# Performance work log

Measured on AMD Instinct MI355X. Metric: run time of the kernel, lower is better.

The kernel has to match this reference:

```python
import jax, jax.numpy as jnp
import numpy as np
from jax import lax

B, S, D, H = 4, 1024, 1024, 16
DK = D // H


def setup_inputs() -> dict:
    key = jax.random.key(0)
    ks = jax.random.split(key, 8)
    s = 0.02
    return {
        "text_embeddings": jax.random.normal(ks[0], (B, S, D), jnp.float32),
        "text_mask": jnp.ones((B, S), jnp.int32),
        "W_G": jax.random.normal(ks[1], (D, D), jnp.float32) * s,
        "b_G": jnp.zeros((D,), jnp.float32),
        "Wq": jax.random.normal(ks[2], (D, D), jnp.float32) * s,
        "bq": jnp.zeros((D,), jnp.float32),
        "Wk": jax.random.normal(ks[3], (D, D), jnp.float32) * s,
        "bk": jnp.zeros((D,), jnp.float32),
        "conv_w": jax.random.normal(ks[4], (D, H, 3), jnp.float32) * s,
        "conv_b": jnp.zeros((D,), jnp.float32),
    }


def _rope_tables(seq_len, dk):
    # interleaved sinusoidal tables, each value repeated twice along feature dim
    pos = jnp.arange(seq_len, dtype=jnp.float32)[:, None]            # [S,1]
    inv = jnp.power(10000.0, -2.0 * jnp.arange(dk // 2, dtype=jnp.float32) / dk)
    ang = pos * inv                                                   # [S,DK/2]
    cos_pos = jnp.repeat(jnp.cos(ang), 2, axis=-1)[None, None]        # [1,1,S,DK]
    sin_pos = jnp.repeat(jnp.sin(ang), 2, axis=-1)[None, None]
    return cos_pos, sin_pos


def reference(text_embeddings, text_mask, W_G, b_G, Wq, bq, Wk, bk, conv_w, conv_b):
    b, s, d = text_embeddings.shape
    g = text_embeddings @ W_G + b_G                                   # [B,S,D]
    q = (g @ Wq + bq).reshape(b, s, H, DK).transpose(0, 2, 1, 3)      # [B,H,S,DK]
    k = (g @ Wk + bk).reshape(b, s, H, DK).transpose(0, 2, 1, 3)

    cos_pos, sin_pos = _rope_tables(s, DK)
    # NOTE: query rotation uses +q_odd (module does NOT negate for q), key uses -k_odd
    qw2 = jnp.stack([q[..., 1::2], q[..., ::2]], axis=-1).reshape(q.shape)
    qw = q * cos_pos + qw2 * sin_pos
    kw2 = jnp.stack([-k[..., 1::2], k[..., ::2]], axis=-1).reshape(k.shape)
    kw = k * cos_pos + kw2 * sin_pos

    scores = jnp.einsum("bhqd,bhkd->bhqk", qw, kw) / np.float32(np.sqrt(DK))
    mask = text_mask[:, None, None, :]                                # [B,1,1,S]
    scores = jnp.where(mask == 0, jnp.float32(-1e9), scores)
    p_attn = jax.nn.softmax(scores, axis=-1)                          # [B,H,S,S]

    row0 = p_attn[:, :, 0, :]                                         # [B,H,S]
    conv = lax.conv_general_dilated(
        row0, conv_w, window_strides=(1,), padding=[(1, 1)],
        dimension_numbers=("NCH", "OIH", "NCH"))                      # [B,D,S]
    return jax.nn.relu(conv + conv_b[None, :, None])
```

## Files before the change

kernel.cpp:

```cpp
#include <hip/hip_runtime.h>
#include <math.h>

#define B_  4
#define S_  1024
#define D_  1024
#define H_  16
#define DK_ 64
#define M_  (B_ * S_)

typedef __bf16 bf16x8 __attribute__((ext_vector_type(8)));
typedef float  f32x4  __attribute__((ext_vector_type(4)));

__device__ __forceinline__ unsigned short f2bf(float f) {
  unsigned u = __builtin_bit_cast(unsigned, f);
  u = (u + 0x7FFFu + ((u >> 16) & 1u)) >> 16;
  return (unsigned short)u;
}
__device__ __forceinline__ float bf2f(unsigned short h) {
  unsigned u = ((unsigned)h) << 16;
  return __builtin_bit_cast(float, u);
}

__device__ __forceinline__ void gl_lds16(const void* g, void* lds) {
  __builtin_amdgcn_global_load_lds(
      (const __attribute__((address_space(1))) unsigned int*)(unsigned long long)g,
      (__attribute__((address_space(3))) unsigned int*)(unsigned int)(unsigned long long)lds,
      16, 0, 0);
}

__global__ __launch_bounds__(256) void prep_kernel(
    const float* __restrict__ X, const float* __restrict__ W_G,
    const float* __restrict__ Wk, unsigned short* __restrict__ Xbf,
    unsigned short* __restrict__ WGT, unsigned short* __restrict__ WkT,
    float* __restrict__ tab) {
  __shared__ float tle[32][33];
  const int blk = blockIdx.x;
  const int tid = threadIdx.x;

  if (blk < 2048) {
    const int i = (blk * 256 + tid) * 2;
    const float4 v0 = ((const float4*)X)[i];
    const float4 v1 = ((const float4*)X)[i + 1];
    ushort4 h0, h1;
    h0.x = f2bf(v0.x); h0.y = f2bf(v0.y); h0.z = f2bf(v0.z); h0.w = f2bf(v0.w);
    h1.x = f2bf(v1.x); h1.y = f2bf(v1.y); h1.z = f2bf(v1.z); h1.w = f2bf(v1.w);
    ((ushort4*)Xbf)[i] = h0;
    ((ushort4*)Xbf)[i + 1] = h1;
  } else if (blk < 4096) {
    const bool isG = blk < 3072;
    const float* W = isG ? W_G : Wk;
    unsigned short* WT = isG ? WGT : WkT;
    const int t = isG ? blk - 2048 : blk - 3072;
    const int k0 = (t & 31) * 32;
    const int n0 = (t >> 5) * 32;
    const int tx = tid & 31;
    const int ty = tid >> 5;
#pragma unroll
    for (int r = 0; r < 32; r += 8)
      tle[ty + r][tx] = W[(size_t)(k0 + ty + r) * 1024 + n0 + tx];
    __syncthreads();
#pragma unroll
    for (int r = 0; r < 32; r += 8)
      WT[(size_t)(n0 + ty + r) * 1024 + k0 + tx] = f2bf(tle[tx][ty + r]);
  } else {
    const int idx = (blk - 4096) * 256 + tid;
    const int s = idx >> 5, j = idx & 31;
    const float inv = (float)exp(-(double)j * (9.210340371976182736 / 32.0));
    float sn, c;
    sincosf((float)s * inv, &sn, &c);
    tab[(size_t)s * 64 + 2 * j] = c;
    tab[(size_t)s * 64 + 2 * j + 1] = sn;
  }
}

#define GM 64
#define GN 128

__global__ __launch_bounds__(256) void gemm_bf16(
    const unsigned short* __restrict__ A, const unsigned short* __restrict__ BT,
    const float* __restrict__ bias, unsigned short* __restrict__ C,
    const float* __restrict__ Wq, float* __restrict__ part, int nGemmBlocks) {
  __shared__ __align__(16) unsigned short As[2][GM * 32];
  __shared__ __align__(16) unsigned short Bs[2][GN * 32];
  __shared__ float gs[4][32];

  const int flat = blockIdx.x;
  const int tid  = threadIdx.x;

  if (flat >= nGemmBlocks) {
    const int qb = flat - nGemmBlocks;
    const int slab = qb >> 2;
    const int n = (qb & 3) * 256 + tid;
    if (tid < 128) {
      const int b = tid >> 5, kk = tid & 31;
      gs[b][kk] = bf2f(A[(size_t)b * S_ * D_ + slab * 32 + kk]);
    }
    __syncthreads();
    float a0 = 0.f, a1 = 0.f, a2 = 0.f, a3 = 0.f;
#pragma unroll
    for (int kk = 0; kk < 32; ++kk) {
      const float w = Wq[(size_t)(slab * 32 + kk) * D_ + n];
      a0 = fmaf(gs[0][kk], w, a0);
      a1 = fmaf(gs[1][kk], w, a1);
      a2 = fmaf(gs[2][kk], w, a2);
      a3 = fmaf(gs[3][kk], w, a3);
    }
    part[(size_t)(slab * 4 + 0) * D_ + n] = a0;
    part[(size_t)(slab * 4 + 1) * D_ + n] = a1;
    part[(size_t)(slab * 4 + 2) * D_ + n] = a2;
    part[(size_t)(slab * 4 + 3) * D_ + n] = a3;
    return;
  }

  const int bx = flat >> 6;
  const int by = flat & 63;
  const int wv   = tid >> 6;
  const int lane = tid & 63;
  const int m0 = by * GM;
  const int n0 = bx * GN;

  const int colOff = (lane & 3) * 8;
  const size_t aOff  = (size_t)(m0 + 16 * wv + (lane >> 2)) * 1024 + colOff;
  const size_t bOff0 = (size_t)(n0 + 32 * wv + (lane >> 2)) * 1024 + colOff;
  const size_t bOff1 = bOff0 + (size_t)16 * 1024;

  const int l15  = lane & 15;
  const int quad = lane >> 4;

  f32x4 acc[4][2];
#pragma unroll
  for (int i = 0; i < 4; ++i)
#pragma unroll
    for (int j = 0; j < 2; ++j) acc[i][j] = (f32x4){0.f, 0.f, 0.f, 0.f};

#pragma unroll 1
  for (int k0 = 0; k0 < 1024; k0 += 64) {
    __syncthreads();
#pragma unroll
    for (int ks = 0; ks < 2; ++ks) {
      gl_lds16(A  + aOff  + k0 + ks * 32, &As[ks][wv * 512]);
      gl_lds16(BT + bOff0 + k0 + ks * 32, &Bs[ks][wv * 1024]);
      gl_lds16(BT + bOff1 + k0 + ks * 32, &Bs[ks][wv * 1024 + 512]);
    }
    __syncthreads();

#pragma unroll
    for (int ks = 0; ks < 2; ++ks) {
      bf16x8 af[4], bfr[2];
#pragma unroll
      for (int mi = 0; mi < 4; ++mi)
        af[mi] = *(const bf16x8*)(&As[ks][(mi * 16 + l15) * 32 + quad * 8]);
#pragma unroll
      for (int ni = 0; ni < 2; ++ni)
        bfr[ni] =
            *(const bf16x8*)(&Bs[ks][(wv * 32 + ni * 16 + l15) * 32 + quad * 8]);
#pragma unroll
      for (int mi = 0; mi < 4; ++mi)
#pragma unroll
        for (int ni = 0; ni < 2; ++ni)
          acc[mi][ni] = __builtin_amdgcn_mfma_f32_16x16x32_bf16(
              af[mi], bfr[ni], acc[mi][ni], 0, 0, 0);
    }
  }

#pragma unroll
  for (int ni = 0; ni < 2; ++ni) {
    const int n = n0 + wv * 32 + ni * 16 + l15;
    const float bv = bias[n];
#pragma unroll
    for (int mi = 0; mi < 4; ++mi) {
#pragma unroll
      for (int r = 0; r < 4; ++r) {
        const int m = m0 + mi * 16 + quad * 4 + r;
        C[(size_t)m * 1024 + n] = f2bf(acc[mi][ni][r] + bv);
      }
    }
  }
}

__global__ __launch_bounds__(256) void attn_scores_kernel(
    const unsigned short* __restrict__ Kbf, const float* __restrict__ part,
    const float* __restrict__ bq, const float* __restrict__ tab,
    const int* __restrict__ mask, float* __restrict__ scores,
    float* __restrict__ mS) {
  const int bi = blockIdx.x;
  const int b = bi >> 9;
  const int h = (bi >> 5) & 15;
  const int chunk = bi & 31;
  const int tid = threadIdx.x;
  const int bh = b * H_ + h;
  const int sl = tid >> 3;
  const int j  = tid & 7;
  const int s  = chunk * 32 + sl;

  __shared__ float q0s[DK_];
  __shared__ float wredm[4];
  __shared__ float wreds[4];

  if (tid < 64) {
    const int n = h * DK_ + tid;
    float v = bq[n];
#pragma unroll
    for (int sl2 = 0; sl2 < 32; ++sl2)
      v += part[(size_t)(sl2 * 4 + b) * D_ + n];
    q0s[tid] = v;
  }
  __syncthreads();

  const ushort4* kp =
      (const ushort4*)(Kbf + ((size_t)(b * S_ + s)) * D_ + h * DK_ + j * 8);
  const ushort4 k0 = kp[0], k1 = kp[1];
  const float4* tb = (const float4*)(tab + (size_t)s * 64 + j * 8);
  const float4 t0 = tb[0], t1 = tb[1];

  float dot = 0.f;
  {
    const float ka = bf2f(k0.x), kb = bf2f(k0.y);
    dot += q0s[j * 8 + 0] * (ka * t0.x - kb * t0.y) +
           q0s[j * 8 + 1] * (kb * t0.x + ka * t0.y);
  }
  {
    const float ka = bf2f(k0.z), kb = bf2f(k0.w);
    dot += q0s[j * 8 + 2] * (ka * t0.z - kb * t0.w) +
           q0s[j * 8 + 3] * (kb * t0.z + ka * t0.w);
  }
  {
    const float ka = bf2f(k1.x), kb = bf2f(k1.y);
    dot += q0s[j * 8 + 4] * (ka * t1.x - kb * t1.y) +
           q0s[j * 8 + 5] * (kb * t1.x + ka * t1.y);
  }
  {
    const float ka = bf2f(k1.z), kb = bf2f(k1.w);
    dot += q0s[j * 8 + 6] * (ka * t1.z - kb * t1.w) +
           q0s[j * 8 + 7] * (kb * t1.z + ka * t1.w);
  }
  dot += __shfl_xor(dot, 1);
  dot += __shfl_xor(dot, 2);
  dot += __shfl_xor(dot, 4);
  dot *= 0.125f;
  if (mask[b * S_ + s] == 0) dot = -1e9f;
  if (j == 0) scores[(size_t)bh * S_ + s] = dot;

  float mx = dot;
#pragma unroll
  for (int off = 8; off < 64; off <<= 1) mx = fmaxf(mx, __shfl_xor(mx, off));
  if ((tid & 63) == 0) wredm[tid >> 6] = mx;
  __syncthreads();
  mx = fmaxf(fmaxf(wredm[0], wredm[1]), fmaxf(wredm[2], wredm[3]));

  float e = (j == 0) ? expf(dot - mx) : 0.f;
#pragma unroll
  for (int off = 1; off < 64; off <<= 1) e += __shfl_xor(e, off);
  if ((tid & 63) == 0) wreds[tid >> 6] = e;
  __syncthreads();
  if (tid == 0) {
    mS[(size_t)(bh * 32 + chunk) * 2 + 0] = mx;
    mS[(size_t)(bh * 32 + chunk) * 2 + 1] =
        wreds[0] + wreds[1] + wreds[2] + wreds[3];
  }
}

__global__ __launch_bounds__(256) void conv_norm_relu_kernel(
    const float* __restrict__ scores, const float* __restrict__ mS,
    const float* __restrict__ cw, const float* __restrict__ cb,
    float* __restrict__ out) {
  const int b  = blockIdx.y;
  const int s0 = blockIdx.x * 128;
  const int o0 = blockIdx.z * 128;
  const int tid = threadIdx.x;
  const int tx = tid & 15;
  const int ty = tid >> 4;

  __shared__ float msh[16], ish[16];
  __shared__ __align__(16) float wT[48][128];
  __shared__ float cbs[128];
  __shared__ __align__(16) float pm[16][132];

  if (tid < 16) {
    const int bh = b * H_ + tid;
    float m = -3e38f;
#pragma unroll
    for (int c = 0; c < 32; ++c)
      m = fmaxf(m, mS[(size_t)(bh * 32 + c) * 2]);
    float S = 0.f;
#pragma unroll
    for (int c = 0; c < 32; ++c)
      S += mS[(size_t)(bh * 32 + c) * 2 + 1] *
           expf(mS[(size_t)(bh * 32 + c) * 2] - m);
    msh[tid] = m;
    ish[tid] = 1.f / S;
  }
  for (int i = tid; i < 128 * 48; i += 256) {
    const int ol = i / 48, ct = i % 48;
    wT[ct][ol] = cw[(size_t)(o0 + ol) * 48 + ct];
  }
  if (tid < 128) cbs[tid] = cb[o0 + tid];
  __syncthreads();

  for (int i = tid; i < 16 * 130; i += 256) {
    const int c = i / 130, ss = i % 130;
    const int gs = s0 - 1 + ss;
    pm[c][ss] = (gs >= 0 && gs < S_)
                    ? expf(scores[(size_t)(b * H_ + c) * S_ + gs] - msh[c]) *
                          ish[c]
                    : 0.f;
  }
  __syncthreads();

  float acc[8][8];
#pragma unroll
  for (int i = 0; i < 8; ++i) {
    const float cv = cbs[ty * 8 + i];
#pragma unroll
    for (int j = 0; j < 8; ++j) acc[i][j] = cv;
  }

#pragma unroll
  for (int c = 0; c < 16; ++c) {
    float p[12];
    *(float4*)(p + 0) = *(const float4*)&pm[c][tx * 8 + 0];
    *(float4*)(p + 4) = *(const float4*)&pm[c][tx * 8 + 4];
    *(float4*)(p + 8) = *(const float4*)&pm[c][tx * 8 + 8];
#pragma unroll
    for (int t = 0; t < 3; ++t) {
      float w[8];
      *(float4*)(w + 0) = *(const float4*)&wT[c * 3 + t][ty * 8 + 0];
      *(float4*)(w + 4) = *(const float4*)&wT[c * 3 + t][ty * 8 + 4];
#pragma unroll
      for (int i = 0; i < 8; ++i)
#pragma unroll
        for (int j = 0; j < 8; ++j)
          acc[i][j] = fmaf(p[j + t], w[i], acc[i][j]);
    }
  }

#pragma unroll
  for (int i = 0; i < 8; ++i) {
    float* orow =
        out + ((size_t)b * D_ + o0 + ty * 8 + i) * S_ + s0 + tx * 8;
    float4 v0, v1;
    v0.x = fmaxf(acc[i][0], 0.f); v0.y = fmaxf(acc[i][1], 0.f);
    v0.z = fmaxf(acc[i][2], 0.f); v0.w = fmaxf(acc[i][3], 0.f);
    v1.x = fmaxf(acc[i][4], 0.f); v1.y = fmaxf(acc[i][5], 0.f);
    v1.z = fmaxf(acc[i][6], 0.f); v1.w = fmaxf(acc[i][7], 0.f);
    *(float4*)(orow + 0) = v0;
    *(float4*)(orow + 4) = v1;
  }
}

extern "C" void kernel_launch(void* const* d_in, const int* in_sizes, int n_in,
                              void* d_out, int out_size, void* d_ws,
                              size_t ws_size, hipStream_t stream) {
  const float* x    = (const float*)d_in[0];
  const int*   mask = (const int*)d_in[1];
  const float* W_G  = (const float*)d_in[2];
  const float* b_G  = (const float*)d_in[3];
  const float* Wq   = (const float*)d_in[4];
  const float* bq   = (const float*)d_in[5];
  const float* Wk   = (const float*)d_in[6];
  const float* bk   = (const float*)d_in[7];
  const float* cw   = (const float*)d_in[8];
  const float* cb   = (const float*)d_in[9];
  float* out = (float*)d_out;

  char* ws = (char*)d_ws;
  unsigned short* Xbf = (unsigned short*)(ws);
  unsigned short* G   = (unsigned short*)(ws + (8u << 20));
  unsigned short* Kbf = (unsigned short*)(ws + (16u << 20));
  unsigned short* WGT = (unsigned short*)(ws + (24u << 20));
  unsigned short* WkT = (unsigned short*)(ws + (26u << 20));
  float* part   = (float*)(ws + (28u << 20));
  float* ropeT  = (float*)(ws + (28u << 20) + (512u << 10));
  float* scores = (float*)(ws + (28u << 20) + (768u << 10));
  float* mS     = (float*)(ws + (28u << 20) + (1024u << 10));

  prep_kernel<<<4224, 256, 0, stream>>>(x, W_G, Wk, Xbf, WGT, WkT, ropeT);
  gemm_bf16<<<512, 256, 0, stream>>>(Xbf, WGT, b_G, G, nullptr, nullptr, 512);
  gemm_bf16<<<640, 256, 0, stream>>>(G, WkT, bk, Kbf, Wq, part, 512);
  attn_scores_kernel<<<2048, 256, 0, stream>>>(Kbf, part, bq, ropeT, mask,
                                               scores, mS);
  conv_norm_relu_kernel<<<dim3(8, B_, 8), 256, 0, stream>>>(
      scores, mS, cw, cb, out);
}
```

Before: 153.4 us.

## Reassociate K projection as X·(W_G·Wk) and compute query row zero directly

The key projection is reassociated as X @ (W_G @ Wk), with the fused bias b_G @ Wk + bk folded in. The two full 4096×1024×1024 GEMMs become one 1024³ weight-product GEMM plus one full GEMM, so G is never materialised. The gated row 0 needed for the query is now computed in fp32 directly from X and W_G in the prep kernel. The GEMM kernel gains tile-index mask/shift parameters and an optional bias. The cost is an extra bf16 rounding of the combined weight matrix, which changes numerical error.

```diff
diff --git a/kernel.cpp b/kernel.cpp
--- a/kernel.cpp
+++ b/kernel.cpp
@@ -30,10 +30,14 @@
 
 __global__ __launch_bounds__(256) void prep_kernel(
     const float* __restrict__ X, const float* __restrict__ W_G,
-    const float* __restrict__ Wk, unsigned short* __restrict__ Xbf,
-    unsigned short* __restrict__ WGT, unsigned short* __restrict__ WkT,
-    float* __restrict__ tab) {
+    const float* __restrict__ Wk, const float* __restrict__ b_G,
+    const float* __restrict__ bk, unsigned short* __restrict__ Xbf,
+    unsigned short* __restrict__ WGbf, unsigned short* __restrict__ WkT,
+    float* __restrict__ tab, float* __restrict__ biask,
+    float* __restrict__ gr0) {
   __shared__ float tle[32][33];
+  __shared__ float xs[1024];
+  __shared__ float pall[256];
   const int blk = blockIdx.x;
   const int tid = threadIdx.x;
 
@@ -46,30 +50,62 @@
     h1.x = f2bf(v1.x); h1.y = f2bf(v1.y); h1.z = f2bf(v1.z); h1.w = f2bf(v1.w);
     ((ushort4*)Xbf)[i] = h0;
     ((ushort4*)Xbf)[i + 1] = h1;
-  } else if (blk < 4096) {
-    const bool isG = blk < 3072;
-    const float* W = isG ? W_G : Wk;
-    unsigned short* WT = isG ? WGT : WkT;
-    const int t = isG ? blk - 2048 : blk - 3072;
+  } else if (blk < 2560) {
+    const int i = ((blk - 2048) * 256 + tid) * 2;
+    const float4 v0 = ((const float4*)W_G)[i];
+    const float4 v1 = ((const float4*)W_G)[i + 1];
+    ushort4 h0, h1;
+    h0.x = f2bf(v0.x); h0.y = f2bf(v0.y); h0.z = f2bf(v0.z); h0.w = f2bf(v0.w);
+    h1.x = f2bf(v1.x); h1.y = f2bf(v1.y); h1.z = f2bf(v1.z); h1.w = f2bf(v1.w);
+    ((ushort4*)WGbf)[i] = h0;
+    ((ushort4*)WGbf)[i + 1] = h1;
+  } else if (blk < 3584) {
+    const int t = blk - 2560;
     const int k0 = (t & 31) * 32;
     const int n0 = (t >> 5) * 32;
     const int tx = tid & 31;
     const int ty = tid >> 5;
 #pragma unroll
     for (int r = 0; r < 32; r += 8)
-      tle[ty + r][tx] = W[(size_t)(k0 + ty + r) * 1024 + n0 + tx];
+      tle[ty + r][tx] = Wk[(size_t)(k0 + ty + r) * 1024 + n0 + tx];
     __syncthreads();
 #pragma unroll
     for (int r = 0; r < 32; r += 8)
-      WT[(size_t)(n0 + ty + r) * 1024 + k0 + tx] = f2bf(tle[tx][ty + r]);
-  } else {
-    const int idx = (blk - 4096) * 256 + tid;
+      WkT[(size_t)(n0 + ty + r) * 1024 + k0 + tx] = f2bf(tle[tx][ty + r]);
+  } else if (blk < 3712) {
+    const int idx = (blk - 3584) * 256 + tid;
     const int s = idx >> 5, j = idx & 31;
     const float inv = (float)exp(-(double)j * (9.210340371976182736 / 32.0));
     float sn, c;
     sincosf((float)s * inv, &sn, &c);
     tab[(size_t)s * 64 + 2 * j] = c;
     tab[(size_t)s * 64 + 2 * j + 1] = sn;
+  } else if (blk < 3716) {
+    const int n = (blk - 3712) * 256 + tid;
+    for (int i = tid; i < 1024; i += 256) xs[i] = b_G[i];
+    __syncthreads();
+    float acc = bk[n];
+    for (int k = 0; k < 1024; ++k)
+      acc = fmaf(xs[k], Wk[(size_t)k * 1024 + n], acc);
+    biask[n] = acc;
+  } else {
+    const int u = blk - 3716;
+    const int b = u >> 4;
+    const int n0g = (u & 15) * 64;
+    const int nl = tid & 63;
+    const int kq = tid >> 6;
+    for (int i = tid; i < 1024; i += 256) xs[i] = X[(size_t)b * S_ * D_ + i];
+    __syncthreads();
+    float acc = 0.f;
+    const int ks = kq * 256;
+    for (int k = ks; k < ks + 256; ++k)
+      acc = fmaf(xs[k], W_G[(size_t)k * 1024 + n0g + nl], acc);
+    pall[tid] = acc;
+    __syncthreads();
+    if (tid < 64)
+      gr0[(size_t)b * 1024 + n0g + tid] = pall[tid] + pall[64 + tid] +
+                                          pall[128 + tid] + pall[192 + tid] +
+                                          b_G[n0g + tid];
   }
 }
 
@@ -79,7 +115,8 @@
 __global__ __launch_bounds__(256) void gemm_bf16(
     const unsigned short* __restrict__ A, const unsigned short* __restrict__ BT,
     const float* __restrict__ bias, unsigned short* __restrict__ C,
-    const float* __restrict__ Wq, float* __restrict__ part, int nGemmBlocks) {
+    const float* __restrict__ gr0, const float* __restrict__ Wq,
+    float* __restrict__ part, int nGemmBlocks, int mtMask, int mtShift) {
   __shared__ __align__(16) unsigned short As[2][GM * 32];
   __shared__ __align__(16) unsigned short Bs[2][GN * 32];
   __shared__ float gs[4][32];
@@ -93,7 +130,7 @@
     const int n = (qb & 3) * 256 + tid;
     if (tid < 128) {
       const int b = tid >> 5, kk = tid & 31;
-      gs[b][kk] = bf2f(A[(size_t)b * S_ * D_ + slab * 32 + kk]);
+      gs[b][kk] = gr0[(size_t)b * 1024 + slab * 32 + kk];
     }
     __syncthreads();
     float a0 = 0.f, a1 = 0.f, a2 = 0.f, a3 = 0.f;
@@ -112,8 +149,8 @@
     return;
   }
 
-  const int bx = flat >> 6;
-  const int by = flat & 63;
+  const int bx = flat >> mtShift;
+  const int by = flat & mtMask;
   const int wv   = tid >> 6;
   const int lane = tid & 63;
   const int m0 = by * GM;
@@ -166,7 +203,7 @@
 #pragma unroll
   for (int ni = 0; ni < 2; ++ni) {
     const int n = n0 + wv * 32 + ni * 16 + l15;
-    const float bv = bias[n];
+    const float bv = bias ? bias[n] : 0.f;
 #pragma unroll
     for (int mi = 0; mi < 4; ++mi) {
 #pragma unroll
@@ -364,19 +401,25 @@
   float* out = (float*)d_out;
 
   char* ws = (char*)d_ws;
-  unsigned short* Xbf = (unsigned short*)(ws);
-  unsigned short* G   = (unsigned short*)(ws + (8u << 20));
-  unsigned short* Kbf = (unsigned short*)(ws + (16u << 20));
-  unsigned short* WGT = (unsigned short*)(ws + (24u << 20));
-  unsigned short* WkT = (unsigned short*)(ws + (26u << 20));
-  float* part   = (float*)(ws + (28u << 20));
-  float* ropeT  = (float*)(ws + (28u << 20) + (512u << 10));
-  float* scores = (float*)(ws + (28u << 20) + (768u << 10));
-  float* mS     = (float*)(ws + (28u << 20) + (1024u << 10));
-
-  prep_kernel<<<4224, 256, 0, stream>>>(x, W_G, Wk, Xbf, WGT, WkT, ropeT);
-  gemm_bf16<<<512, 256, 0, stream>>>(Xbf, WGT, b_G, G, nullptr, nullptr, 512);
-  gemm_bf16<<<640, 256, 0, stream>>>(G, WkT, bk, Kbf, Wq, part, 512);
+  unsigned short* Xbf  = (unsigned short*)(ws);
+  unsigned short* Kbf  = (unsigned short*)(ws + (8u << 20));
+  unsigned short* WkT  = (unsigned short*)(ws + (16u << 20));
+  unsigned short* WGbf = (unsigned short*)(ws + (18u << 20));
+  unsigned short* WcT  = (unsigned short*)(ws + (20u << 20));
+  char* base2 = ws + (22u << 20);
+  float* gr0    = (float*)(base2);
+  float* biask  = (float*)(base2 + (16u << 10));
+  float* part   = (float*)(base2 + (20u << 10));
+  float* ropeT  = (float*)(base2 + (532u << 10));
+  float* scores = (float*)(base2 + (788u << 10));
+  float* mS     = (float*)(base2 + (1044u << 10));
+
+  prep_kernel<<<3780, 256, 0, stream>>>(x, W_G, Wk, b_G, bk, Xbf, WGbf, WkT,
+                                        ropeT, biask, gr0);
+  gemm_bf16<<<256, 256, 0, stream>>>(WkT, WGbf, nullptr, WcT, gr0, Wq, part,
+                                     128, 15, 4);
+  gemm_bf16<<<512, 256, 0, stream>>>(Xbf, WcT, biask, Kbf, nullptr, nullptr,
+                                     nullptr, 512, 63, 6);
   attn_scores_kernel<<<2048, 256, 0, stream>>>(Kbf, part, bq, ropeT, mask,
                                                scores, mS);
   conv_norm_relu_kernel<<<dim3(8, B_, 8), 256, 0, stream>>>(
```

New measurement: 206.0 us. 34.3% more time.
